# Performance work log

Hardware: AMD Instinct MI355X
Metric: run time of the kernel (lower is better)

## Reference

```python
import jax, jax.numpy as jnp
import numpy as np

B, C, HH, WW = 2, 64, 56, 56
NH, IP, OP = 4, 32, 64  # num_heads, inter_plane, out_plane
EPS = 1e-5


def setup_inputs() -> dict:
    key = jax.random.key(0)
    ks = jax.random.split(key, 12)
    r = lambda k, sh, s: jax.random.normal(k, sh, jnp.float32) * s
    inp = {
        "x": r(ks[0], (B, C, HH, WW), 1.0),
        # 1x1 conv QKV projections: weight [out_ch, in_ch], kaiming-ish scale
        "wk": r(ks[1], (NH * IP, C), C ** -0.5), "bk": jnp.zeros((NH * IP,), jnp.float32),
        "wq": r(ks[2], (NH * IP, C), C ** -0.5), "bq": jnp.zeros((NH * IP,), jnp.float32),
        "wv": r(ks[3], (NH * IP, C), C ** -0.5), "bv": jnp.zeros((NH * IP,), jnp.float32),
        # GCN linears
        "w1": r(ks[4], (OP, IP), IP ** -0.5), "b1": jnp.zeros((OP,), jnp.float32),
        "g1": 1.0 + r(ks[5], (NH * OP,), 0.1), "be1": jnp.zeros((NH * OP,), jnp.float32),
        "rm1": jnp.zeros((NH * OP,), jnp.float32), "rv1": jnp.ones((NH * OP,), jnp.float32),
        "w2": r(ks[6], (OP, OP), OP ** -0.5), "b2": jnp.zeros((OP,), jnp.float32),
        "g2": 1.0 + r(ks[7], (NH * OP,), 0.1), "be2": jnp.zeros((NH * OP,), jnp.float32),
        "rm2": jnp.zeros((NH * OP,), jnp.float32), "rv2": jnp.ones((NH * OP,), jnp.float32),
        # final 1x1 projection
        "wf": r(ks[8], (OP, NH * OP), (NH * OP) ** -0.5), "bf": jnp.zeros((OP,), jnp.float32),
    }
    return inp


def _conv1x1(x, w, b):
    # x: [b,c,h,w], w: [o,c] -> [b,o,h,w]
    return jnp.einsum('bchw,oc->bohw', x, w) + b[None, :, None, None]


def _bn_relu(y, g, be, rm, rv, b, n):
    # y: [b,H,N,OP]; BatchNorm1d(H*OP) in eval mode over channel axis, then ReLU
    z = y.transpose(0, 1, 3, 2).reshape(b, NH * OP, n)  # [b, H*OP, N]
    z = (z - rm[None, :, None]) * (g / jnp.sqrt(rv + EPS))[None, :, None] + be[None, :, None]
    return jax.nn.relu(z.reshape(b, NH, OP, n).transpose(0, 1, 3, 2))  # [b,H,N,OP]


def reference(x, wk, bk, wq, bq, wv, bv, w1, b1, g1, be1, rm1, rv1,
              w2, b2, g2, be2, rm2, rv2, wf, bf):
    b, c, h, w = x.shape
    n = h * w
    node_k = _conv1x1(x, wk, bk).reshape(b, NH, IP, n).transpose(0, 1, 3, 2)  # [b,H,N,IP]
    node_q = _conv1x1(x, wq, bq).reshape(b, NH, IP, n)                        # [b,H,IP,N]
    node_v = _conv1x1(x, wv, bv).reshape(b, NH, IP, n).transpose(0, 1, 3, 2)  # [b,H,N,IP]
    adj = jnp.einsum('bhnd,bhdm->bhnm', node_k, node_q)  # [b,H,N,N]
    adj = jax.nn.softmax(adj, axis=2)  # NOTE: torch softmax(dim=2) -> normalize over rows axis
    av = jnp.einsum('bhnm,bhmd->bhnd', adj, node_v)      # [b,H,N,IP]
    avw = _bn_relu(av @ w1.T + b1, g1, be1, rm1, rv1, b, n)   # [b,H,N,OP]; dropout is identity (eval)
    av2 = jnp.einsum('bhnm,bhmd->bhnd', adj, avw)        # [b,H,N,OP]
    avw2 = _bn_relu(av2 @ w2.T + b2, g2, be2, rm2, rv2, b, n)  # [b,H,N,OP]
    y = avw2.transpose(0, 1, 3, 2).reshape(b, NH * OP, h, w)
    return _conv1x1(y, wf, bf)  # [b, OP, h, w]
```

## Files before the change

kernel.cpp:

```cpp
#include <hip/hip_runtime.h>
#include <hip/hip_bf16.h>

typedef __hip_bfloat16 bf16;
typedef __attribute__((ext_vector_type(8))) short bfrag;
typedef __attribute__((ext_vector_type(4))) short s16x4;
typedef __attribute__((ext_vector_type(4))) float f32x4;
typedef __attribute__((ext_vector_type(16))) float f32x16;

#define MFMA32(a,b,c) __builtin_amdgcn_mfma_f32_32x32x16_bf16((a),(b),(c),0,0,0)

__device__ __forceinline__ float b2f(bf16 x){ return __bfloat162float(x); }
__device__ __forceinline__ bf16 f2b(float x){ return __float2bfloat16(x); }
__device__ __forceinline__ float fexp2(float x){ return __builtin_amdgcn_exp2f(x); }
__device__ __forceinline__ float us2f(unsigned short u){ unsigned v = (unsigned)u << 16; return __uint_as_float(v); }

#define NN   3136
#define NBH  8
#define NCH  7
#define MCH  448
#define LDP  40
#define LDPA 72
#define LDW  272
#define LOG2E 1.44269504f

__global__ __launch_bounds__(256) void k_zero(float* __restrict__ p, int n4)
{
    int i = blockIdx.x * 256 + threadIdx.x;
    if (i < n4) reinterpret_cast<f32x4*>(p)[i] = (f32x4){0.f, 0.f, 0.f, 0.f};
}

__global__ __launch_bounds__(256) void k_proj(
    const float* __restrict__ x,
    const float* __restrict__ wk, const float* __restrict__ bk,
    const float* __restrict__ wq, const float* __restrict__ bq,
    const float* __restrict__ wv, const float* __restrict__ bv,
    bf16* __restrict__ kt, bf16* __restrict__ qt, bf16* __restrict__ vt)
{
    __shared__ __align__(16) bf16 xT[32 * 72];
    __shared__ __align__(16) bf16 wT[128 * 72];
    int tid = threadIdx.x, w = tid >> 6, lane = tid & 63;
    int l31 = lane & 31, lsel = lane >> 5;
    int n0 = blockIdx.x * 32;
    int p  = blockIdx.y;
    int b  = blockIdx.z;
    const float* wp = (p == 0) ? wk : ((p == 1) ? wq : wv);
    const float* bp = (p == 0) ? bk : ((p == 1) ? bq : bv);

    for (int i = tid; i < 2048; i += 256) {
        int c = i >> 5, j = i & 31;
        xT[j * 72 + c] = f2b(x[((size_t)b * 64 + c) * NN + n0 + j]);
    }
    for (int i = tid; i < 8192; i += 256) {
        int oc = i >> 6, c = i & 63;
        wT[oc * 72 + c] = f2b(wp[oc * 64 + c]);
    }
    __syncthreads();

    f32x16 s;
    #pragma unroll
    for (int r = 0; r < 16; ++r) s[r] = 0.f;
    #pragma unroll
    for (int k = 0; k < 4; ++k) {
        bfrag a  = *(const bfrag*)(&xT[l31 * 72 + k * 16 + lsel * 8]);
        bfrag bw = *(const bfrag*)(&wT[(w * 32 + l31) * 72 + k * 16 + lsel * 8]);
        s = MFMA32(a, bw, s);
    }
    float bias = bp[w * 32 + l31];
    size_t bh = (size_t)b * 4 + w;
    if (p == 2) {
        #pragma unroll
        for (int q = 0; q < 4; ++q) {
            s16x4 pk;
            #pragma unroll
            for (int i = 0; i < 4; ++i) {
                bf16 e = f2b(s[4 * q + i] + bias);
                pk[i] = *(short*)&e;
            }
            *(s16x4*)(vt + (bh * 32 + l31) * NN + n0 + 8 * q + 4 * lsel) = pk;
        }
    } else {
        bf16* dst = (p == 0) ? kt : qt;
        float sc = (p == 0) ? LOG2E : 1.0f;
        #pragma unroll
        for (int r = 0; r < 16; ++r) {
            int nl = (r & 3) + 8 * (r >> 2) + 4 * lsel;
            dst[(bh * NN + n0 + nl) * 32 + l31] = f2b((s[r] + bias) * sc);
        }
    }
}

__global__ __launch_bounds__(256) void k_stats(const bf16* __restrict__ kt,
                                               const bf16* __restrict__ qt,
                                               float* __restrict__ den)
{
    __shared__ __align__(16) bf16 Kb[2][64 * LDP];
    int tid = threadIdx.x, w = tid >> 6, lane = tid & 63;
    int l31 = lane & 31, lsel = lane >> 5;
    int bh = blockIdx.z;
    int mt = blockIdx.x * 4 + w;
    bool act = (mt < 98);
    int m0 = (act ? mt : 97) * 32;
    int ns = blockIdx.y * MCH;

    const bf16* qp = qt + ((size_t)bh * NN + m0 + l31) * 32 + lsel * 8;
    bfrag qb0 = *(const bfrag*)qp;
    bfrag qb1 = *(const bfrag*)(qp + 16);
    const bf16* kt_bh = kt + (size_t)bh * NN * 32;

    int sr = tid >> 2, sc = (tid & 3) * 8;
    const bf16* sbase = kt_bh + (size_t)(ns + sr) * 32 + sc;
    int soff = sr * LDP + sc;

    *(bfrag*)(&Kb[0][soff]) = *(const bfrag*)sbase;
    __syncthreads();

    float dacc = 0.f;
    for (int t = 0; t < 7; ++t) {
        bfrag pre;
        bool hn = (t + 1 < 7);
        if (hn) pre = *(const bfrag*)(sbase + (size_t)(t + 1) * 2048);
        const bf16* kl = &Kb[t & 1][0];
        #pragma unroll
        for (int nt = 0; nt < 2; ++nt) {
            int ko = (l31 + 32 * nt) * LDP + lsel * 8;
            bfrag kb0 = *(const bfrag*)(kl + ko);
            bfrag kb1 = *(const bfrag*)(kl + ko + 16);
            f32x16 s;
            #pragma unroll
            for (int r = 0; r < 16; ++r) s[r] = 0.f;
            s = MFMA32(kb0, qb0, s);
            s = MFMA32(kb1, qb1, s);
            float ps = 0.f;
            #pragma unroll
            for (int r = 0; r < 16; ++r) ps += fexp2(s[r]);
            dacc += ps;
        }
        if (hn) *(bfrag*)(&Kb[(t + 1) & 1][soff]) = pre;
        __syncthreads();
    }
    dacc += __shfl_xor(dacc, 32);
    if (act && lane < 32) atomicAdd(&den[(size_t)bh * NN + m0 + l31], dacc);
}

__global__ __launch_bounds__(256) void k_recip(float* __restrict__ den)
{
    int i = blockIdx.x * 256 + threadIdx.x;
    if (i < NBH * NN) den[i] = 1.0f / den[i];
}

__global__ __launch_bounds__(256) void k_scalev(bf16* __restrict__ vt, const float* __restrict__ rden)
{
    int by = blockIdx.y;
    const float* rdp = rden + ((size_t)(by >> 5)) * NN;
    bf16* vp = vt + (size_t)by * NN;
    int i = blockIdx.x * 256 + threadIdx.x;
    if (i < 392) {
        int m = i * 8;
        union { bfrag v; unsigned short us[8]; } u;
        u.v = *(const bfrag*)(vp + m);
        #pragma unroll
        for (int j = 0; j < 8; ++j) {
            bf16 e = f2b(us2f(u.us[j]) * rdp[m + j]);
            u.us[j] = *(unsigned short*)&e;
        }
        *(bfrag*)(vp + m) = u.v;
    }
}

__global__ __launch_bounds__(256) void k_av(const bf16* __restrict__ kt,
    const bf16* __restrict__ qt, const bf16* __restrict__ vtp,
    bf16* __restrict__ av_p)
{
    __shared__ __align__(16) bf16 Qb[2][64 * LDP];
    __shared__ __align__(16) bf16 Vb[2][32 * LDPA];
    int tid = threadIdx.x, w = tid >> 6, lane = tid & 63;
    int l31 = lane & 31, lsel = lane >> 5;
    int bh = blockIdx.z;
    int ntile = blockIdx.x * 4 + w;
    bool act = (ntile < 98);
    int n0 = (act ? ntile : 97) * 32;
    int ms = blockIdx.y * MCH;

    const bf16* kp = kt + ((size_t)bh * NN + n0 + l31) * 32 + lsel * 8;
    bfrag kb0 = *(const bfrag*)kp;
    bfrag kb1 = *(const bfrag*)(kp + 16);
    const bf16* qt_bh = qt + (size_t)bh * NN * 32;
    const bf16* vt_bh = vtp + (size_t)bh * 32 * NN;

    int qr = tid >> 2, qc = (tid & 3) * 8;
    const bf16* qsb = qt_bh + (size_t)(ms + qr) * 32 + qc;
    int qoff = qr * LDP + qc;
    int vr = tid >> 3, vc = (tid & 7) * 8;
    const bf16* vsb = vt_bh + (size_t)vr * NN + ms + vc;
    int voff = vr * LDPA + vc;

    *(bfrag*)(&Qb[0][qoff]) = *(const bfrag*)qsb;
    *(bfrag*)(&Vb[0][voff]) = *(const bfrag*)vsb;
    __syncthreads();

    f32x16 acc;
    #pragma unroll
    for (int r = 0; r < 16; ++r) acc[r] = 0.f;

    for (int t = 0; t < 7; ++t) {
        bfrag preQ, preV;
        bool hn = (t + 1 < 7);
        if (hn) {
            preQ = *(const bfrag*)(qsb + (size_t)(t + 1) * 2048);
            preV = *(const bfrag*)(vsb + (size_t)(t + 1) * 64);
        }
        const bf16* ql = &Qb[t & 1][0];
        const bf16* vl = &Vb[t & 1][0];
        #pragma unroll
        for (int mt2 = 0; mt2 < 2; ++mt2) {
            int qo = (l31 + 32 * mt2) * LDP + lsel * 8;
            bfrag q0 = *(const bfrag*)(ql + qo);
            bfrag q1 = *(const bfrag*)(ql + qo + 16);
            f32x16 s;
            #pragma unroll
            for (int r = 0; r < 16; ++r) s[r] = 0.f;
            s = MFMA32(q0, kb0, s);
            s = MFMA32(q1, kb1, s);
            union { unsigned short us[8]; bfrag v; } pa0, pa1;
            #pragma unroll
            for (int i = 0; i < 8; ++i) {
                bf16 e0 = f2b(fexp2(s[i]));
                bf16 e1 = f2b(fexp2(s[8 + i]));
                pa0.us[i] = *(unsigned short*)&e0;
                pa1.us[i] = *(unsigned short*)&e1;
            }
            const bf16* vrow = vl + l31 * LDPA + 32 * mt2 + lsel * 4;
            union { s16x4 h[2]; bfrag v; } vb0, vb1;
            vb0.h[0] = *(const s16x4*)(vrow);
            vb0.h[1] = *(const s16x4*)(vrow + 8);
            vb1.h[0] = *(const s16x4*)(vrow + 16);
            vb1.h[1] = *(const s16x4*)(vrow + 24);
            acc = MFMA32(pa0.v, vb0.v, acc);
            acc = MFMA32(pa1.v, vb1.v, acc);
        }
        if (hn) {
            *(bfrag*)(&Qb[(t + 1) & 1][qoff]) = preQ;
            *(bfrag*)(&Vb[(t + 1) & 1][voff]) = preV;
        }
        __syncthreads();
    }
    if (act) {
        bf16* dst = av_p + (size_t)blockIdx.y * ((size_t)NBH * NN * 32)
                  + ((size_t)bh * NN + n0) * 32 + l31;
        #pragma unroll
        for (int r = 0; r < 16; ++r) {
            int nl = (r & 3) + 8 * (r >> 2) + 4 * lsel;
            dst[(size_t)nl * 32] = f2b(acc[r]);
        }
    }
}

__global__ __launch_bounds__(256) void k_av2(const bf16* __restrict__ kt,
    const bf16* __restrict__ qt, const bf16* __restrict__ awts,
    bf16* __restrict__ av2_p)
{
    __shared__ __align__(16) bf16 Qb[2][64 * LDP];
    __shared__ __align__(16) bf16 Ab[2][64 * LDPA];
    int tid = threadIdx.x, w = tid >> 6, lane = tid & 63;
    int l31 = lane & 31, lsel = lane >> 5;
    int bh = blockIdx.z;
    int ntile = blockIdx.x * 4 + w;
    bool act = (ntile < 98);
    int n0 = (act ? ntile : 97) * 32;
    int ms = blockIdx.y * MCH;

    const bf16* kp = kt + ((size_t)bh * NN + n0 + l31) * 32 + lsel * 8;
    bfrag kb0 = *(const bfrag*)kp;
    bfrag kb1 = *(const bfrag*)(kp + 16);
    const bf16* qt_bh = qt + (size_t)bh * NN * 32;
    const bf16* aw_bh = awts + (size_t)bh * 64 * NN;

    int qr = tid >> 2, qc = (tid & 3) * 8;
    const bf16* qsb = qt_bh + (size_t)(ms + qr) * 32 + qc;
    int qoff = qr * LDP + qc;
    int ar0 = tid >> 3, acv = (tid & 7) * 8;
    const bf16* asb0 = aw_bh + (size_t)ar0 * NN + ms + acv;
    const bf16* asb1 = aw_bh + (size_t)(ar0 + 32) * NN + ms + acv;
    int aoff0 = ar0 * LDPA + acv;
    int aoff1 = (ar0 + 32) * LDPA + acv;

    *(bfrag*)(&Qb[0][qoff])  = *(const bfrag*)qsb;
    *(bfrag*)(&Ab[0][aoff0]) = *(const bfrag*)asb0;
    *(bfrag*)(&Ab[0][aoff1]) = *(const bfrag*)asb1;
    __syncthreads();

    f32x16 acc0, acc1;
    #pragma unroll
    for (int r = 0; r < 16; ++r) { acc0[r] = 0.f; acc1[r] = 0.f; }

    for (int t = 0; t < 7; ++t) {
        bfrag preQ, preA0, preA1;
        bool hn = (t + 1 < 7);
        if (hn) {
            preQ  = *(const bfrag*)(qsb  + (size_t)(t + 1) * 2048);
            preA0 = *(const bfrag*)(asb0 + (size_t)(t + 1) * 64);
            preA1 = *(const bfrag*)(asb1 + (size_t)(t + 1) * 64);
        }
        const bf16* ql = &Qb[t & 1][0];
        const bf16* al = &Ab[t & 1][0];
        #pragma unroll
        for (int mt2 = 0; mt2 < 2; ++mt2) {
            int qo = (l31 + 32 * mt2) * LDP + lsel * 8;
            bfrag q0 = *(const bfrag*)(ql + qo);
            bfrag q1 = *(const bfrag*)(ql + qo + 16);
            f32x16 s;
            #pragma unroll
            for (int r = 0; r < 16; ++r) s[r] = 0.f;
            s = MFMA32(q0, kb0, s);
            s = MFMA32(q1, kb1, s);
            union { unsigned short us[8]; bfrag v; } pa0, pa1;
            #pragma unroll
            for (int i = 0; i < 8; ++i) {
                bf16 e0 = f2b(fexp2(s[i]));
                bf16 e1 = f2b(fexp2(s[8 + i]));
                pa0.us[i] = *(unsigned short*)&e0;
                pa1.us[i] = *(unsigned short*)&e1;
            }
            const bf16* a0 = al + l31 * LDPA + 32 * mt2 + lsel * 4;
            const bf16* a1 = al + (l31 + 32) * LDPA + 32 * mt2 + lsel * 4;
            union { s16x4 h[2]; bfrag v; } e00, e01, e10, e11;
            e00.h[0] = *(const s16x4*)(a0);
            e00.h[1] = *(const s16x4*)(a0 + 8);
            e01.h[0] = *(const s16x4*)(a0 + 16);
            e01.h[1] = *(const s16x4*)(a0 + 24);
            e10.h[0] = *(const s16x4*)(a1);
            e10.h[1] = *(const s16x4*)(a1 + 8);
            e11.h[0] = *(const s16x4*)(a1 + 16);
            e11.h[1] = *(const s16x4*)(a1 + 24);
            acc0 = MFMA32(pa0.v, e00.v, acc0);
            acc0 = MFMA32(pa1.v, e01.v, acc0);
            acc1 = MFMA32(pa0.v, e10.v, acc1);
            acc1 = MFMA32(pa1.v, e11.v, acc1);
        }
        if (hn) {
            *(bfrag*)(&Qb[(t + 1) & 1][qoff])  = preQ;
            *(bfrag*)(&Ab[(t + 1) & 1][aoff0]) = preA0;
            *(bfrag*)(&Ab[(t + 1) & 1][aoff1]) = preA1;
        }
        __syncthreads();
    }
    if (act) {
        bf16* dst = av2_p + (size_t)blockIdx.y * ((size_t)NBH * NN * 64)
                  + ((size_t)bh * NN + n0) * 64 + l31;
        #pragma unroll
        for (int r = 0; r < 16; ++r) {
            int nl = (r & 3) + 8 * (r >> 2) + 4 * lsel;
            dst[(size_t)nl * 64]      = f2b(acc0[r]);
            dst[(size_t)nl * 64 + 32] = f2b(acc1[r]);
        }
    }
}

__global__ __launch_bounds__(256) void k_red1(const bf16* __restrict__ av_p,
    const float* __restrict__ w1, const float* __restrict__ b1,
    const float* __restrict__ g1, const float* __restrict__ be1,
    const float* __restrict__ rm1, const float* __restrict__ rv1,
    const float* __restrict__ rds,
    bf16* __restrict__ awts)
{
    __shared__ float avl[64 * 33];
    __shared__ float w1l[64 * 33];
    __shared__ float sc[64], sh[64], bb[64];
    int n0 = blockIdx.x * 64, bh = blockIdx.y, h = bh & 3;
    int tid = threadIdx.x;
    const size_t cstride = (size_t)NBH * NN * 32;
    const bf16* ap = av_p + ((size_t)bh * NN + n0) * 32;
    {
        int nr = tid >> 2, e8 = (tid & 3) * 8;
        int base = nr * 32 + e8;
        float s8[8];
        #pragma unroll
        for (int j = 0; j < 8; ++j) s8[j] = 0.f;
        #pragma unroll
        for (int c = 0; c < NCH; ++c) {
            union { bfrag v; unsigned short us[8]; } u;
            u.v = *(const bfrag*)(ap + (size_t)c * cstride + base);
            #pragma unroll
            for (int j = 0; j < 8; ++j) s8[j] += us2f(u.us[j]);
        }
        #pragma unroll
        for (int j = 0; j < 8; ++j) avl[nr * 33 + e8 + j] = s8[j];
    }
    for (int i = tid; i < 2048; i += 256)
        w1l[(i >> 5) * 33 + (i & 31)] = w1[i];
    if (tid < 64) {
        int ch = h * 64 + tid;
        float s = g1[ch] * rsqrtf(rv1[ch] + 1e-5f);
        sc[tid] = s; sh[tid] = be1[ch] - rm1[ch] * s; bb[tid] = b1[tid];
    }
    __syncthreads();
    int nb = (tid & 15) * 4, eb = (tid >> 4) * 4;
    float rsc[4];
    {
        const float* rp = rds + (size_t)bh * NN + n0 + nb;
        rsc[0] = rp[0]; rsc[1] = rp[1]; rsc[2] = rp[2]; rsc[3] = rp[3];
    }
    float s[4][4];
    #pragma unroll
    for (int i = 0; i < 4; ++i)
        #pragma unroll
        for (int j = 0; j < 4; ++j) s[i][j] = bb[eb + j];
    for (int d = 0; d < 32; ++d) {
        float a0 = avl[(nb+0)*33+d], a1 = avl[(nb+1)*33+d], a2 = avl[(nb+2)*33+d], a3 = avl[(nb+3)*33+d];
        float w0 = w1l[(eb+0)*33+d], w1v = w1l[(eb+1)*33+d], w2v = w1l[(eb+2)*33+d], w3 = w1l[(eb+3)*33+d];
        s[0][0]+=a0*w0; s[0][1]+=a0*w1v; s[0][2]+=a0*w2v; s[0][3]+=a0*w3;
        s[1][0]+=a1*w0; s[1][1]+=a1*w1v; s[1][2]+=a1*w2v; s[1][3]+=a1*w3;
        s[2][0]+=a2*w0; s[2][1]+=a2*w1v; s[2][2]+=a2*w2v; s[2][3]+=a2*w3;
        s[3][0]+=a3*w0; s[3][1]+=a3*w1v; s[3][2]+=a3*w2v; s[3][3]+=a3*w3;
    }
    #pragma unroll
    for (int j = 0; j < 4; ++j) {
        int e = eb + j;
        ushort4 pk;
        float v0 = fmaxf(s[0][j] * sc[e] + sh[e], 0.f) * rsc[0];
        float v1 = fmaxf(s[1][j] * sc[e] + sh[e], 0.f) * rsc[1];
        float v2 = fmaxf(s[2][j] * sc[e] + sh[e], 0.f) * rsc[2];
        float v3 = fmaxf(s[3][j] * sc[e] + sh[e], 0.f) * rsc[3];
        bf16 b0 = f2b(v0), b1b = f2b(v1), b2b = f2b(v2), b3 = f2b(v3);
        pk.x = *(unsigned short*)&b0; pk.y = *(unsigned short*)&b1b;
        pk.z = *(unsigned short*)&b2b; pk.w = *(unsigned short*)&b3;
        *reinterpret_cast<ushort4*>(awts + ((size_t)bh * 64 + e) * NN + n0 + nb) = pk;
    }
}

__global__ __launch_bounds__(256) void k_red2(const bf16* __restrict__ av2_p,
    const float* __restrict__ w2, const float* __restrict__ b2,
    const float* __restrict__ g2, const float* __restrict__ be2,
    const float* __restrict__ rm2, const float* __restrict__ rv2,
    bf16* __restrict__ yt)
{
    __shared__ float a2l[64 * 65];
    __shared__ float w2l[64 * 65];
    __shared__ float sc[64], sh[64], bb[64];
    int n0 = blockIdx.x * 64, bh = blockIdx.y, h = bh & 3, b = bh >> 2;
    int tid = threadIdx.x;
    const size_t cstride = (size_t)NBH * NN * 64;
    const bf16* ap = av2_p + ((size_t)bh * NN + n0) * 64;
    #pragma unroll
    for (int it = 0; it < 2; ++it) {
        int idx = it * 256 + tid;
        int nr = idx >> 3, e8 = (idx & 7) * 8;
        int base = nr * 64 + e8;
        float s8[8];
        #pragma unroll
        for (int j = 0; j < 8; ++j) s8[j] = 0.f;
        #pragma unroll
        for (int c = 0; c < NCH; ++c) {
            union { bfrag v; unsigned short us[8]; } u;
            u.v = *(const bfrag*)(ap + (size_t)c * cstride + base);
            #pragma unroll
            for (int j = 0; j < 8; ++j) s8[j] += us2f(u.us[j]);
        }
        #pragma unroll
        for (int j = 0; j < 8; ++j) a2l[nr * 65 + e8 + j] = s8[j];
    }
    for (int i = tid; i < 4096; i += 256)
        w2l[(i >> 6) * 65 + (i & 63)] = w2[i];
    if (tid < 64) {
        int ch = h * 64 + tid;
        float s = g2[ch] * rsqrtf(rv2[ch] + 1e-5f);
        sc[tid] = s; sh[tid] = be2[ch] - rm2[ch] * s; bb[tid] = b2[tid];
    }
    __syncthreads();
    int nb = (tid & 15) * 4, eb = (tid >> 4) * 4;
    float s[4][4];
    #pragma unroll
    for (int i = 0; i < 4; ++i)
        #pragma unroll
        for (int j = 0; j < 4; ++j) s[i][j] = bb[eb + j];
    for (int d = 0; d < 64; ++d) {
        float a0 = a2l[(nb+0)*65+d], a1 = a2l[(nb+1)*65+d], a2 = a2l[(nb+2)*65+d], a3 = a2l[(nb+3)*65+d];
        float w0 = w2l[(eb+0)*65+d], w1v = w2l[(eb+1)*65+d], w2v = w2l[(eb+2)*65+d], w3 = w2l[(eb+3)*65+d];
        s[0][0]+=a0*w0; s[0][1]+=a0*w1v; s[0][2]+=a0*w2v; s[0][3]+=a0*w3;
        s[1][0]+=a1*w0; s[1][1]+=a1*w1v; s[1][2]+=a1*w2v; s[1][3]+=a1*w3;
        s[2][0]+=a2*w0; s[2][1]+=a2*w1v; s[2][2]+=a2*w2v; s[2][3]+=a2*w3;
        s[3][0]+=a3*w0; s[3][1]+=a3*w1v; s[3][2]+=a3*w2v; s[3][3]+=a3*w3;
    }
    #pragma unroll
    for (int i = 0; i < 4; ++i) {
        ushort4 pk;
        float v0 = fmaxf(s[i][0] * sc[eb+0] + sh[eb+0], 0.f);
        float v1 = fmaxf(s[i][1] * sc[eb+1] + sh[eb+1], 0.f);
        float v2 = fmaxf(s[i][2] * sc[eb+2] + sh[eb+2], 0.f);
        float v3 = fmaxf(s[i][3] * sc[eb+3] + sh[eb+3], 0.f);
        bf16 b0 = f2b(v0), b1b = f2b(v1), b2b = f2b(v2), b3 = f2b(v3);
        pk.x = *(unsigned short*)&b0; pk.y = *(unsigned short*)&b1b;
        pk.z = *(unsigned short*)&b2b; pk.w = *(unsigned short*)&b3;
        *reinterpret_cast<ushort4*>(yt + ((size_t)b * NN + n0 + nb + i) * 256 + h * 64 + eb) = pk;
    }
}

__global__ __launch_bounds__(256) void k_finalM(const bf16* __restrict__ yt,
    const float* __restrict__ wf, const float* __restrict__ bf_,
    float* __restrict__ out)
{
    __shared__ __align__(16) bf16 wfb[32 * LDW];
    __shared__ float red[4 * 16 * 64];
    int tid = threadIdx.x, w = tid >> 6, lane = tid & 63;
    int l31 = lane & 31, lsel = lane >> 5;
    int n0 = blockIdx.x * 32;
    int b  = blockIdx.y;
    int o0 = blockIdx.z * 32;

    for (int i = tid; i < 8192; i += 256) {
        int o = i >> 8, k = i & 255;
        wfb[o * LDW + k] = f2b(wf[(size_t)(o0 + o) * 256 + k]);
    }
    __syncthreads();

    const bf16* yb = yt + ((size_t)b * NN + n0 + l31) * 256 + w * 64 + lsel * 8;
    const bf16* wb = &wfb[l31 * LDW + w * 64 + lsel * 8];
    f32x16 s;
    #pragma unroll
    for (int r = 0; r < 16; ++r) s[r] = 0.f;
    #pragma unroll
    for (int kk = 0; kk < 4; ++kk) {
        bfrag a  = *(const bfrag*)(wb + kk * 16);
        bfrag bv = *(const bfrag*)(yb + kk * 16);
        s = MFMA32(a, bv, s);
    }
    float* rp = &red[(w * 16) * 64 + lane];
    #pragma unroll
    for (int r = 0; r < 16; ++r) rp[r * 64] = s[r];
    __syncthreads();

    for (int idx = tid; idx < 1024; idx += 256) {
        int ln = idx & 63, r = idx >> 6;
        float v = red[r * 64 + ln] + red[(16 + r) * 64 + ln]
                + red[(32 + r) * 64 + ln] + red[(48 + r) * 64 + ln];
        int ol = (r & 3) + 8 * (r >> 2) + 4 * (ln >> 5);
        int o = o0 + ol;
        out[((size_t)b * 64 + o) * NN + n0 + (ln & 31)] = v + bf_[o];
    }
}

extern "C" void kernel_launch(void* const* d_in, const int* in_sizes, int n_in,
                              void* d_out, int out_size, void* d_ws, size_t ws_size,
                              hipStream_t stream)
{
    const float* x   = (const float*)d_in[0];
    const float* wk  = (const float*)d_in[1];
    const float* bk  = (const float*)d_in[2];
    const float* wq  = (const float*)d_in[3];
    const float* bq  = (const float*)d_in[4];
    const float* wv  = (const float*)d_in[5];
    const float* bv  = (const float*)d_in[6];
    const float* w1  = (const float*)d_in[7];
    const float* b1  = (const float*)d_in[8];
    const float* g1  = (const float*)d_in[9];
    const float* be1 = (const float*)d_in[10];
    const float* rm1 = (const float*)d_in[11];
    const float* rv1 = (const float*)d_in[12];
    const float* w2  = (const float*)d_in[13];
    const float* b2  = (const float*)d_in[14];
    const float* g2  = (const float*)d_in[15];
    const float* be2 = (const float*)d_in[16];
    const float* rm2 = (const float*)d_in[17];
    const float* rv2 = (const float*)d_in[18];
    const float* wf  = (const float*)d_in[19];
    const float* bff = (const float*)d_in[20];
    float* out = (float*)d_out;

    char* ws = (char*)d_ws;
    bf16* kt   = (bf16*)ws;
    bf16* qt   = kt + (size_t)NBH * NN * 32;
    bf16* vt   = qt + (size_t)NBH * NN * 32;
    bf16* awts = vt + (size_t)NBH * 32 * NN;
    bf16* yt   = awts + (size_t)NBH * 64 * NN;
    float* den = (float*)(yt + (size_t)2 * NN * 256);
    bf16* av_p  = (bf16*)(den + (size_t)NBH * NN);
    bf16* av2_p = av_p + (size_t)NCH * NBH * NN * 32;

    k_zero  <<<dim3(25),       256, 0, stream>>>(den, 6272);
    k_proj  <<<dim3(98, 3, 2), 256, 0, stream>>>(x, wk, bk, wq, bq, wv, bv, kt, qt, vt);
    k_stats <<<dim3(25, 7, 8), 256, 0, stream>>>(kt, qt, den);
    k_recip <<<dim3(98),       256, 0, stream>>>(den);
    k_scalev<<<dim3(2, 256),   256, 0, stream>>>(vt, den);
    k_av    <<<dim3(25, 7, 8), 256, 0, stream>>>(kt, qt, vt, av_p);
    k_red1  <<<dim3(49, 8),    256, 0, stream>>>(av_p, w1, b1, g1, be1, rm1, rv1, den, awts);
    k_av2   <<<dim3(25, 7, 8), 256, 0, stream>>>(kt, qt, awts, av2_p);
    k_red2  <<<dim3(49, 8),    256, 0, stream>>>(av2_p, w2, b2, g2, be2, rm2, rv2, yt);
    k_finalM<<<dim3(98, 2, 2), 256, 0, stream>>>(yt, wf, bff, out);
}
```

Before: 103.9 us.

## Process two query tiles per wave in stats kernel, halve reduction-kernel tiles

The softmax-denominator kernel now has each wave handle two 32-column query tiles against each shared-memory K chunk, which halves the number of blocks and the K reload traffic. The two linear+BN reduction kernels now process 32 nodes per block instead of 64, doubling the block count to improve occupancy and parallelism. In red1, half the threads load the partial sums while the other half load the weights. Costs include more registers per wave in the stats kernel and more redundant weight loads across the reduction blocks.

Result: no change. 104.8 us (+0.8%).

```diff
diff --git a/kernel.cpp b/kernel.cpp
--- a/kernel.cpp
+++ b/kernel.cpp
@@ -97,14 +97,19 @@
     int tid = threadIdx.x, w = tid >> 6, lane = tid & 63;
     int l31 = lane & 31, lsel = lane >> 5;
     int bh = blockIdx.z;
-    int mt = blockIdx.x * 4 + w;
-    bool act = (mt < 98);
-    int m0 = (act ? mt : 97) * 32;
+    int mtA = blockIdx.x * 8 + w * 2;
+    int mtB = mtA + 1;
+    bool actA = (mtA < 98), actB = (mtB < 98);
+    int m0A = (actA ? mtA : 97) * 32;
+    int m0B = (actB ? mtB : 97) * 32;
     int ns = blockIdx.y * MCH;
 
-    const bf16* qp = qt + ((size_t)bh * NN + m0 + l31) * 32 + lsel * 8;
-    bfrag qb0 = *(const bfrag*)qp;
-    bfrag qb1 = *(const bfrag*)(qp + 16);
+    const bf16* qpA = qt + ((size_t)bh * NN + m0A + l31) * 32 + lsel * 8;
+    bfrag qbA0 = *(const bfrag*)qpA;
+    bfrag qbA1 = *(const bfrag*)(qpA + 16);
+    const bf16* qpB = qt + ((size_t)bh * NN + m0B + l31) * 32 + lsel * 8;
+    bfrag qbB0 = *(const bfrag*)qpB;
+    bfrag qbB1 = *(const bfrag*)(qpB + 16);
     const bf16* kt_bh = kt + (size_t)bh * NN * 32;
 
     int sr = tid >> 2, sc = (tid & 3) * 8;
@@ -114,7 +119,7 @@
     *(bfrag*)(&Kb[0][soff]) = *(const bfrag*)sbase;
     __syncthreads();
 
-    float dacc = 0.f;
+    float dA = 0.f, dB = 0.f;
     for (int t = 0; t < 7; ++t) {
         bfrag pre;
         bool hn = (t + 1 < 7);
@@ -125,21 +130,38 @@
             int ko = (l31 + 32 * nt) * LDP + lsel * 8;
             bfrag kb0 = *(const bfrag*)(kl + ko);
             bfrag kb1 = *(const bfrag*)(kl + ko + 16);
-            f32x16 s;
-            #pragma unroll
-            for (int r = 0; r < 16; ++r) s[r] = 0.f;
-            s = MFMA32(kb0, qb0, s);
-            s = MFMA32(kb1, qb1, s);
-            float ps = 0.f;
-            #pragma unroll
-            for (int r = 0; r < 16; ++r) ps += fexp2(s[r]);
-            dacc += ps;
+            {
+                f32x16 s;
+                #pragma unroll
+                for (int r = 0; r < 16; ++r) s[r] = 0.f;
+                s = MFMA32(kb0, qbA0, s);
+                s = MFMA32(kb1, qbA1, s);
+                float ps = 0.f;
+                #pragma unroll
+                for (int r = 0; r < 16; ++r) ps += fexp2(s[r]);
+                dA += ps;
+            }
+            {
+                f32x16 s;
+                #pragma unroll
+                for (int r = 0; r < 16; ++r) s[r] = 0.f;
+                s = MFMA32(kb0, qbB0, s);
+                s = MFMA32(kb1, qbB1, s);
+                float ps = 0.f;
+                #pragma unroll
+                for (int r = 0; r < 16; ++r) ps += fexp2(s[r]);
+                dB += ps;
+            }
         }
         if (hn) *(bfrag*)(&Kb[(t + 1) & 1][soff]) = pre;
         __syncthreads();
     }
-    dacc += __shfl_xor(dacc, 32);
-    if (act && lane < 32) atomicAdd(&den[(size_t)bh * NN + m0 + l31], dacc);
+    dA += __shfl_xor(dA, 32);
+    dB += __shfl_xor(dB, 32);
+    if (lane < 32) {
+        if (actA) atomicAdd(&den[(size_t)bh * NN + m0A + l31], dA);
+        if (actB) atomicAdd(&den[(size_t)bh * NN + m0B + l31], dB);
+    }
 }
 
 __global__ __launch_bounds__(256) void k_recip(float* __restrict__ den)
@@ -363,14 +385,14 @@
     const float* __restrict__ rds,
     bf16* __restrict__ awts)
 {
-    __shared__ float avl[64 * 33];
+    __shared__ float avl[32 * 33];
     __shared__ float w1l[64 * 33];
     __shared__ float sc[64], sh[64], bb[64];
-    int n0 = blockIdx.x * 64, bh = blockIdx.y, h = bh & 3;
+    int n0 = blockIdx.x * 32, bh = blockIdx.y, h = bh & 3;
     int tid = threadIdx.x;
     const size_t cstride = (size_t)NBH * NN * 32;
     const bf16* ap = av_p + ((size_t)bh * NN + n0) * 32;
-    {
+    if (tid < 128) {
         int nr = tid >> 2, e8 = (tid & 3) * 8;
         int base = nr * 32 + e8;
         float s8[8];
@@ -385,36 +407,35 @@
         }
         #pragma unroll
         for (int j = 0; j < 8; ++j) avl[nr * 33 + e8 + j] = s8[j];
-    }
-    for (int i = tid; i < 2048; i += 256)
-        w1l[(i >> 5) * 33 + (i & 31)] = w1[i];
+    } else {
+        for (int i = tid - 128; i < 2048; i += 128)
+            w1l[(i >> 5) * 33 + (i & 31)] = w1[i];
+    }
     if (tid < 64) {
         int ch = h * 64 + tid;
         float s = g1[ch] * rsqrtf(rv1[ch] + 1e-5f);
         sc[tid] = s; sh[tid] = be1[ch] - rm1[ch] * s; bb[tid] = b1[tid];
     }
     __syncthreads();
-    int nb = (tid & 15) * 4, eb = (tid >> 4) * 4;
+    int nb = (tid & 7) * 4, eb = (tid >> 3) * 2;
     float rsc[4];
     {
         const float* rp = rds + (size_t)bh * NN + n0 + nb;
         rsc[0] = rp[0]; rsc[1] = rp[1]; rsc[2] = rp[2]; rsc[3] = rp[3];
     }
-    float s[4][4];
-    #pragma unroll
-    for (int i = 0; i < 4; ++i)
-        #pragma unroll
-        for (int j = 0; j < 4; ++j) s[i][j] = bb[eb + j];
+    float s[4][2];
+    #pragma unroll
+    for (int i = 0; i < 4; ++i) { s[i][0] = bb[eb]; s[i][1] = bb[eb + 1]; }
     for (int d = 0; d < 32; ++d) {
         float a0 = avl[(nb+0)*33+d], a1 = avl[(nb+1)*33+d], a2 = avl[(nb+2)*33+d], a3 = avl[(nb+3)*33+d];
-        float w0 = w1l[(eb+0)*33+d], w1v = w1l[(eb+1)*33+d], w2v = w1l[(eb+2)*33+d], w3 = w1l[(eb+3)*33+d];
-        s[0][0]+=a0*w0; s[0][1]+=a0*w1v; s[0][2]+=a0*w2v; s[0][3]+=a0*w3;
-        s[1][0]+=a1*w0; s[1][1]+=a1*w1v; s[1][2]+=a1*w2v; s[1][3]+=a1*w3;
-        s[2][0]+=a2*w0; s[2][1]+=a2*w1v; s[2][2]+=a2*w2v; s[2][3]+=a2*w3;
-        s[3][0]+=a3*w0; s[3][1]+=a3*w1v; s[3][2]+=a3*w2v; s[3][3]+=a3*w3;
-    }
-    #pragma unroll
-    for (int j = 0; j < 4; ++j) {
+        float w0 = w1l[(eb+0)*33+d], w1v = w1l[(eb+1)*33+d];
+        s[0][0]+=a0*w0; s[0][1]+=a0*w1v;
+        s[1][0]+=a1*w0; s[1][1]+=a1*w1v;
+        s[2][0]+=a2*w0; s[2][1]+=a2*w1v;
+        s[3][0]+=a3*w0; s[3][1]+=a3*w1v;
+    }
+    #pragma unroll
+    for (int j = 0; j < 2; ++j) {
         int e = eb + j;
         ushort4 pk;
         float v0 = fmaxf(s[0][j] * sc[e] + sh[e], 0.f) * rsc[0];
@@ -434,17 +455,15 @@
     const float* __restrict__ rm2, const float* __restrict__ rv2,
     bf16* __restrict__ yt)
 {
-    __shared__ float a2l[64 * 65];
+    __shared__ float a2l[32 * 65];
     __shared__ float w2l[64 * 65];
     __shared__ float sc[64], sh[64], bb[64];
-    int n0 = blockIdx.x * 64, bh = blockIdx.y, h = bh & 3, b = bh >> 2;
+    int n0 = blockIdx.x * 32, bh = blockIdx.y, h = bh & 3, b = bh >> 2;
     int tid = threadIdx.x;
     const size_t cstride = (size_t)NBH * NN * 64;
     const bf16* ap = av2_p + ((size_t)bh * NN + n0) * 64;
-    #pragma unroll
-    for (int it = 0; it < 2; ++it) {
-        int idx = it * 256 + tid;
-        int nr = idx >> 3, e8 = (idx & 7) * 8;
+    {
+        int nr = tid >> 3, e8 = (tid & 7) * 8;
         int base = nr * 64 + e8;
         float s8[8];
         #pragma unroll
@@ -467,31 +486,27 @@
         sc[tid] = s; sh[tid] = be2[ch] - rm2[ch] * s; bb[tid] = b2[tid];
     }
     __syncthreads();
-    int nb = (tid & 15) * 4, eb = (tid >> 4) * 4;
-    float s[4][4];
-    #pragma unroll
-    for (int i = 0; i < 4; ++i)
-        #pragma unroll
-        for (int j = 0; j < 4; ++j) s[i][j] = bb[eb + j];
+    int nb = (tid & 7) * 4, eb = (tid >> 3) * 2;
+    float s[4][2];
+    #pragma unroll
+    for (int i = 0; i < 4; ++i) { s[i][0] = bb[eb]; s[i][1] = bb[eb + 1]; }
     for (int d = 0; d < 64; ++d) {
         float a0 = a2l[(nb+0)*65+d], a1 = a2l[(nb+1)*65+d], a2 = a2l[(nb+2)*65+d], a3 = a2l[(nb+3)*65+d];
-        float w0 = w2l[(eb+0)*65+d], w1v = w2l[(eb+1)*65+d], w2v = w2l[(eb+2)*65+d], w3 = w2l[(eb+3)*65+d];
-        s[0][0]+=a0*w0; s[0][1]+=a0*w1v; s[0][2]+=a0*w2v; s[0][3]+=a0*w3;
-        s[1][0]+=a1*w0; s[1][1]+=a1*w1v; s[1][2]+=a1*w2v; s[1][3]+=a1*w3;
-        s[2][0]+=a2*w0; s[2][1]+=a2*w1v; s[2][2]+=a2*w2v; s[2][3]+=a2*w3;
-        s[3][0]+=a3*w0; s[3][1]+=a3*w1v; s[3][2]+=a3*w2v; s[3][3]+=a3*w3;
+        float w0 = w2l[(eb+0)*65+d], w1v = w2l[(eb+1)*65+d];
+        s[0][0]+=a0*w0; s[0][1]+=a0*w1v;
+        s[1][0]+=a1*w0; s[1][1]+=a1*w1v;
+        s[2][0]+=a2*w0; s[2][1]+=a2*w1v;
+        s[3][0]+=a3*w0; s[3][1]+=a3*w1v;
     }
     #pragma unroll
     for (int i = 0; i < 4; ++i) {
-        ushort4 pk;
-        float v0 = fmaxf(s[i][0] * sc[eb+0] + sh[eb+0], 0.f);
+        float v0 = fmaxf(s[i][0] * sc[eb]   + sh[eb],   0.f);
         float v1 = fmaxf(s[i][1] * sc[eb+1] + sh[eb+1], 0.f);
-        float v2 = fmaxf(s[i][2] * sc[eb+2] + sh[eb+2], 0.f);
-        float v3 = fmaxf(s[i][3] * sc[eb+3] + sh[eb+3], 0.f);
-        bf16 b0 = f2b(v0), b1b = f2b(v1), b2b = f2b(v2), b3 = f2b(v3);
-        pk.x = *(unsigned short*)&b0; pk.y = *(unsigned short*)&b1b;
-        pk.z = *(unsigned short*)&b2b; pk.w = *(unsigned short*)&b3;
-        *reinterpret_cast<ushort4*>(yt + ((size_t)b * NN + n0 + nb + i) * 256 + h * 64 + eb) = pk;
+        union { unsigned u; unsigned short us[2]; } pk2;
+        bf16 e0 = f2b(v0), e1 = f2b(v1);
+        pk2.us[0] = *(unsigned short*)&e0;
+        pk2.us[1] = *(unsigned short*)&e1;
+        *reinterpret_cast<unsigned*>(yt + ((size_t)b * NN + n0 + nb + i) * 256 + h * 64 + eb) = pk2.u;
     }
 }
 
@@ -578,12 +593,12 @@
 
     k_zero  <<<dim3(25),       256, 0, stream>>>(den, 6272);
     k_proj  <<<dim3(98, 3, 2), 256, 0, stream>>>(x, wk, bk, wq, bq, wv, bv, kt, qt, vt);
-    k_stats <<<dim3(25, 7, 8), 256, 0, stream>>>(kt, qt, den);
+    k_stats <<<dim3(13, 7, 8), 256, 0, stream>>>(kt, qt, den);
     k_recip <<<dim3(98),       256, 0, stream>>>(den);
     k_scalev<<<dim3(2, 256),   256, 0, stream>>>(vt, den);
     k_av    <<<dim3(25, 7, 8), 256, 0, stream>>>(kt, qt, vt, av_p);
-    k_red1  <<<dim3(49, 8),    256, 0, stream>>>(av_p, w1, b1, g1, be1, rm1, rv1, den, awts);
+    k_red1  <<<dim3(98, 8),    256, 0, stream>>>(av_p, w1, b1, g1, be1, rm1, rv1, den, awts);
     k_av2   <<<dim3(25, 7, 8), 256, 0, stream>>>(kt, qt, awts, av2_p);
-    k_red2  <<<dim3(49, 8),    256, 0, stream>>>(av2_p, w2, b2, g2, be2, rm2, rv2, yt);
+    k_red2  <<<dim3(98, 8),    256, 0, stream>>>(av2_p, w2, b2, g2, be2, rm2, rv2, yt);
     k_finalM<<<dim3(98, 2, 2), 256, 0, stream>>>(yt, wf, bff, out);
 }
```
